# Optimization experiments

Measured on AMD Instinct MI355X. Metric: run time of the kernel, lower is better.

Reference implementation:

```python
import jax, jax.numpy as jnp
import numpy as np

H = 64  # hidden_size
IN = 1  # input_size
OUT = 32  # fc output


def _lstm_layer(x, Wih, Whh, bih, bhh):
    """x: (B,T,D_in). Returns (outputs (B,T,H), final h (B,H)). PyTorch gate order i,f,g,o."""
    B = x.shape[0]
    b = bih + bhh  # (4H,)
    # precompute input contributions for all timesteps: (T,B,4H)
    xW = jnp.einsum('btd,gd->tbg', x, Wih) + b

    def step(carry, xw_t):
        h, c = carry
        gates = xw_t + h @ Whh.T  # (B,4H)
        i, f, g, o = jnp.split(gates, 4, axis=-1)
        i = jax.nn.sigmoid(i)
        f = jax.nn.sigmoid(f)
        g = jnp.tanh(g)
        o = jax.nn.sigmoid(o)
        c = f * c + i * g
        h = o * jnp.tanh(c)
        return (h, c), h

    h0 = jnp.zeros((B, H), dtype=x.dtype)
    c0 = jnp.zeros((B, H), dtype=x.dtype)
    (h_T, _), hs = jax.lax.scan(step, (h0, c0), xW)
    return jnp.swapaxes(hs, 0, 1), h_T


def setup_inputs() -> dict:
    key = jax.random.key(0)
    ks = jax.random.split(key, 11)
    s_ih0 = 1.0 / np.sqrt(H)
    inp = {
        'x': jax.random.normal(ks[0], (2048, 512, IN), dtype=jnp.float32),
        # layer 0: input_size -> H
        'Wih0': jax.random.uniform(ks[1], (4 * H, IN), minval=-s_ih0, maxval=s_ih0),
        'Whh0': jax.random.uniform(ks[2], (4 * H, H), minval=-s_ih0, maxval=s_ih0),
        'bih0': jax.random.uniform(ks[3], (4 * H,), minval=-s_ih0, maxval=s_ih0),
        'bhh0': jax.random.uniform(ks[4], (4 * H,), minval=-s_ih0, maxval=s_ih0),
        # layer 1: H -> H
        'Wih1': jax.random.uniform(ks[5], (4 * H, H), minval=-s_ih0, maxval=s_ih0),
        'Whh1': jax.random.uniform(ks[6], (4 * H, H), minval=-s_ih0, maxval=s_ih0),
        'bih1': jax.random.uniform(ks[7], (4 * H,), minval=-s_ih0, maxval=s_ih0),
        'bhh1': jax.random.uniform(ks[8], (4 * H,), minval=-s_ih0, maxval=s_ih0),
        # fc: H -> 32
        'fcW': jax.random.uniform(ks[9], (OUT, H), minval=-s_ih0, maxval=s_ih0),
        'fcb': jax.random.uniform(ks[10], (OUT,), minval=-s_ih0, maxval=s_ih0),
    }
    return inp


def reference(x, Wih0, Whh0, bih0, bhh0, Wih1, Whh1, bih1, bhh1, fcW, fcb):
    h1_seq, _ = _lstm_layer(x, Wih0, Whh0, bih0, bhh0)
    _, h_last = _lstm_layer(h1_seq, Wih1, Whh1, bih1, bhh1)  # hidden[-1]
    features = jax.nn.relu(h_last @ fcW.T + fcb)  # (B, 32)
    return features
```

## Files before the change

### kernel.cpp

```cpp
#include <hip/hip_runtime.h>
#include <hip/hip_bf16.h>


#define HID 64
#define TSTEPS 512
#define MB 8
#define RS 80

typedef _Float16 f16x8 __attribute__((ext_vector_type(8)));
typedef float f32x4 __attribute__((ext_vector_type(4)));
typedef float f32x2 __attribute__((ext_vector_type(2)));

#define KSIG (-1.44269504089f)
#define KTANH (2.88539008178f)

__device__ __forceinline__ f32x2 mk2(float a, float b) { f32x2 r; r[0] = a; r[1] = b; return r; }
__device__ __forceinline__ f32x2 exp2v(f32x2 v) {
    f32x2 r; r[0] = __builtin_amdgcn_exp2f(v[0]); r[1] = __builtin_amdgcn_exp2f(v[1]); return r;
}
__device__ __forceinline__ f32x2 rcpv(f32x2 v) {
    f32x2 r; r[0] = __builtin_amdgcn_rcpf(v[0]); r[1] = __builtin_amdgcn_rcpf(v[1]); return r;
}
__device__ __forceinline__ f32x2 sig2(f32x2 p)  { return rcpv(exp2v(p) + 1.0f); }
__device__ __forceinline__ f32x2 tanh2(f32x2 p) { return 1.0f - 2.0f * rcpv(exp2v(p) + 1.0f); }

__global__ __launch_bounds__(512, 1) void lstm_feat_kernel(
    const float* __restrict__ x,
    const float* __restrict__ Wih0, const float* __restrict__ Whh0,
    const float* __restrict__ bih0, const float* __restrict__ bhh0,
    const float* __restrict__ Wih1, const float* __restrict__ Whh1,
    const float* __restrict__ bih1, const float* __restrict__ bhh1,
    const float* __restrict__ fcW, const float* __restrict__ fcb,
    float* __restrict__ out)
{
    __shared__ float x_lds[(MB / 2) * TSTEPS * 2];
    __shared__ __align__(16) _Float16 h0_lds[2][MB * RS];
    __shared__ __align__(16) _Float16 h1_lds[2][MB * RS];
    __shared__ float h1f32[MB * HID];
    __shared__ float fcw_lds[HID * 32];
    __shared__ float fcb_lds[32];

    const int tid  = threadIdx.x;
    const int wave = tid >> 6;
    const int lane = tid & 63;
    const int nq   = lane & 15;
    const int quad = lane >> 4;
    const int bbase = blockIdx.x * MB;
    const bool isL1 = (wave >= 4);
    const int ug = wave & 3;
    const int u  = ug * 16 + nq;

    for (int i = tid; i < TSTEPS * MB; i += 512) {
        int r = i >> 9, t = i & (TSTEPS - 1);
        x_lds[(r >> 1) * (TSTEPS * 2) + t * 2 + (r & 1)] = x[(bbase + r) * TSTEPS + t];
    }
    for (int i = tid; i < 32 * HID; i += 512) {
        int o = i >> 6, kk = i & 63;
        fcw_lds[kk * 32 + o] = fcW[i];
    }
    if (tid < 32) fcb_lds[tid] = fcb[tid];
    for (int i = tid; i < 2 * MB * RS; i += 512) {
        ((_Float16*)h0_lds)[i] = (_Float16)0.f;
        ((_Float16*)h1_lds)[i] = (_Float16)0.f;
    }

    f16x8 wA[4][2], wB[4][2];
    f32x4 cbias[4];
    float wx0s[4];
    {
        const float* Wa = isL1 ? Wih1 : Whh0;
        const float* Wb = isL1 ? Whh1 : Whh0;
        const float* bi = isL1 ? bih1 : bih0;
        const float* bh = isL1 ? bhh1 : bhh0;
        #pragma unroll
        for (int g = 0; g < 4; ++g) {
            const float sc = (g == 2) ? KTANH : KSIG;
            const int n = g * 64 + u;
            const float bs = (bi[n] + bh[n]) * sc;
            cbias[g] = (f32x4){bs, bs, bs, bs};
            wx0s[g] = Wih0[n] * sc;
            #pragma unroll
            for (int ks = 0; ks < 2; ++ks) {
                const int k0 = quad * 8 + ks * 32;
                f16x8 a, b;
                #pragma unroll
                for (int j = 0; j < 8; ++j) {
                    a[j] = (_Float16)(Wa[n * HID + k0 + j] * sc);
                    b[j] = (_Float16)(Wb[n * HID + k0 + j] * sc);
                }
                wA[g][ks] = a; wB[g][ks] = b;
            }
        }
    }

    const f32x4 zero4 = {0.f, 0.f, 0.f, 0.f};
    const int arow = (nq >> 1) * RS + quad * 8;
    const int b0r  = (quad * 2) * RS;
    const int hbase = quad * 2;
    f32x2 cc = mk2(0.f, 0.f);

    __syncthreads();

#define L0_SUB(P, Q, XQ2) do {                                                       \
    f16x8 a0_ = *(const f16x8*)&h0_lds[P][arow];                                     \
    f16x8 a1_ = *(const f16x8*)&h0_lds[P][arow + 32];                                \
    f32x4 ac[4];                                                                     \
    __builtin_amdgcn_s_setprio(1);                                                   \
    _Pragma("unroll")                                                                \
    for (int g = 0; g < 4; ++g)                                                      \
        ac[g] = __builtin_amdgcn_mfma_f32_16x16x32_f16(a0_, wA[g][0], cbias[g], 0, 0, 0); \
    _Pragma("unroll")                                                                \
    for (int g = 0; g < 4; ++g)                                                      \
        ac[g] = __builtin_amdgcn_mfma_f32_16x16x32_f16(a1_, wA[g][1], ac[g], 0, 0, 0); \
    __builtin_amdgcn_s_setprio(0);                                                   \
    f32x2 pi = (XQ2) * wx0s[0] + mk2(ac[0][0], ac[0][2]);                            \
    f32x2 pf = (XQ2) * wx0s[1] + mk2(ac[1][0], ac[1][2]);                            \
    f32x2 pg = (XQ2) * wx0s[2] + mk2(ac[2][0], ac[2][2]);                            \
    f32x2 po = (XQ2) * wx0s[3] + mk2(ac[3][0], ac[3][2]);                            \
    f32x2 iv = sig2(pi), fv = sig2(pf), gv = tanh2(pg), ov = sig2(po);               \
    cc = fv * cc + iv * gv;                                                          \
    f32x2 hh = ov * tanh2(cc * KTANH);                                               \
    h0_lds[Q][b0r + u]      = (_Float16)hh[0];                                       \
    h0_lds[Q][b0r + RS + u] = (_Float16)hh[1];                                       \
} while (0)

#define L1_SUB(P, Q, GUARD) do {                                                     \
    f16x8 a00 = *(const f16x8*)&h0_lds[P][arow];                                     \
    f16x8 a01 = *(const f16x8*)&h0_lds[P][arow + 32];                                \
    f16x8 a10 = *(const f16x8*)&h1_lds[P][arow];                                     \
    f16x8 a11 = *(const f16x8*)&h1_lds[P][arow + 32];                                \
    f32x4 aA[4], aB[4];                                                              \
    __builtin_amdgcn_s_setprio(1);                                                   \
    _Pragma("unroll")                                                                \
    for (int g = 0; g < 4; ++g)                                                      \
        aA[g] = __builtin_amdgcn_mfma_f32_16x16x32_f16(a00, wA[g][0], zero4, 0, 0, 0); \
    _Pragma("unroll")                                                                \
    for (int g = 0; g < 4; ++g)                                                      \
        aB[g] = __builtin_amdgcn_mfma_f32_16x16x32_f16(a10, wB[g][0], cbias[g], 0, 0, 0); \
    _Pragma("unroll")                                                                \
    for (int g = 0; g < 4; ++g)                                                      \
        aA[g] = __builtin_amdgcn_mfma_f32_16x16x32_f16(a01, wA[g][1], aA[g], 0, 0, 0); \
    _Pragma("unroll")                                                                \
    for (int g = 0; g < 4; ++g)                                                      \
        aB[g] = __builtin_amdgcn_mfma_f32_16x16x32_f16(a11, wB[g][1], aB[g], 0, 0, 0); \
    __builtin_amdgcn_s_setprio(0);                                                   \
    if (GUARD) {                                                                     \
        f32x2 pi = mk2(aA[0][0], aA[0][2]) + mk2(aB[0][0], aB[0][2]);                \
        f32x2 pf = mk2(aA[1][0], aA[1][2]) + mk2(aB[1][0], aB[1][2]);                \
        f32x2 pg = mk2(aA[2][0], aA[2][2]) + mk2(aB[2][0], aB[2][2]);                \
        f32x2 po = mk2(aA[3][0], aA[3][2]) + mk2(aB[3][0], aB[3][2]);                \
        f32x2 iv = sig2(pi), fv = sig2(pf), gv = tanh2(pg), ov = sig2(po);           \
        cc = fv * cc + iv * gv;                                                      \
        f32x2 hh = ov * tanh2(cc * KTANH);                                           \
        h1_lds[Q][b0r + u]      = (_Float16)hh[0];                                   \
        h1_lds[Q][b0r + RS + u] = (_Float16)hh[1];                                   \
    }                                                                                \
} while (0)

    const int xoff = quad * (TSTEPS * 2);
    for (int k = 0; k < TSTEPS; k += 2) {
        f32x2 xa, xb;
        if (!isL1) {
            const f32x4 xv = *(const f32x4*)&x_lds[xoff + k * 2];
            xa = mk2(xv[0], xv[1]); xb = mk2(xv[2], xv[3]);
            L0_SUB(0, 1, xa);
        } else {
            L1_SUB(0, 1, (k > 0));
        }
        __syncthreads();
        if (!isL1) {
            L0_SUB(1, 0, xb);
        } else {
            L1_SUB(1, 0, true);
        }
        __syncthreads();
    }

    if (isL1) {
        f16x8 a00 = *(const f16x8*)&h0_lds[0][arow];
        f16x8 a01 = *(const f16x8*)&h0_lds[0][arow + 32];
        f16x8 a10 = *(const f16x8*)&h1_lds[0][arow];
        f16x8 a11 = *(const f16x8*)&h1_lds[0][arow + 32];
        f32x4 aA[4], aB[4];
        #pragma unroll
        for (int g = 0; g < 4; ++g)
            aA[g] = __builtin_amdgcn_mfma_f32_16x16x32_f16(a00, wA[g][0], zero4, 0, 0, 0);
        #pragma unroll
        for (int g = 0; g < 4; ++g)
            aB[g] = __builtin_amdgcn_mfma_f32_16x16x32_f16(a10, wB[g][0], cbias[g], 0, 0, 0);
        #pragma unroll
        for (int g = 0; g < 4; ++g)
            aA[g] = __builtin_amdgcn_mfma_f32_16x16x32_f16(a01, wA[g][1], aA[g], 0, 0, 0);
        #pragma unroll
        for (int g = 0; g < 4; ++g)
            aB[g] = __builtin_amdgcn_mfma_f32_16x16x32_f16(a11, wB[g][1], aB[g], 0, 0, 0);
        f32x2 pi = mk2(aA[0][0], aA[0][2]) + mk2(aB[0][0], aB[0][2]);
        f32x2 pf = mk2(aA[1][0], aA[1][2]) + mk2(aB[1][0], aB[1][2]);
        f32x2 pg = mk2(aA[2][0], aA[2][2]) + mk2(aB[2][0], aB[2][2]);
        f32x2 po = mk2(aA[3][0], aA[3][2]) + mk2(aB[3][0], aB[3][2]);
        f32x2 iv = sig2(pi), fv = sig2(pf), gv = tanh2(pg), ov = sig2(po);
        cc = fv * cc + iv * gv;
        f32x2 hh = ov * tanh2(cc * KTANH);
        h1f32[hbase * HID + u]       = hh[0];
        h1f32[(hbase + 1) * HID + u] = hh[1];
    }
    __syncthreads();

    if (tid < MB * 32) {
        const int o  = tid & 31;
        const int rr = tid >> 5;
        float acc = fcb_lds[o];
        #pragma unroll 8
        for (int kk = 0; kk < HID; ++kk)
            acc += h1f32[rr * HID + kk] * fcw_lds[kk * 32 + o];
        out[(bbase + rr) * 32 + o] = fmaxf(acc, 0.f);
    }
}

extern "C" void kernel_launch(void* const* d_in, const int* in_sizes, int n_in,
                              void* d_out, int out_size, void* d_ws, size_t ws_size,
                              hipStream_t stream) {
    const float* x    = (const float*)d_in[0];
    const float* Wih0 = (const float*)d_in[1];
    const float* Whh0 = (const float*)d_in[2];
    const float* bih0 = (const float*)d_in[3];
    const float* bhh0 = (const float*)d_in[4];
    const float* Wih1 = (const float*)d_in[5];
    const float* Whh1 = (const float*)d_in[6];
    const float* bih1 = (const float*)d_in[7];
    const float* bhh1 = (const float*)d_in[8];
    const float* fcW  = (const float*)d_in[9];
    const float* fcb  = (const float*)d_in[10];
    float* out = (float*)d_out;

    lstm_feat_kernel<<<2048 / MB, 512, 0, stream>>>(
        x, Wih0, Whh0, bih0, bhh0, Wih1, Whh1, bih1, bhh1, fcW, fcb, out);
}
```

Before: 316.0 us.

## Lag layer-1 by two steps and precompute its input projection off the critical path

Layer 1 now runs two timesteps behind layer 0, with a four-deep h0 ring buffer. The Wih1·h0 projection for a later step is computed after the recurrent MFMAs and carried in accumulator registers, so only the Whh1 chain sits on the dependent path. Layer 0 folds the x·Wih0 term into the MFMA accumulator init instead of adding it afterwards, and the loop is unrolled by four with scalar activations. In exchange it uses more LDS and accumulator registers and needs extra prologue and epilogue steps to drain the lag.

Result: no change. 312.7 us (-1.0%).

```diff
diff --git a/kernel.cpp b/kernel.cpp
--- a/kernel.cpp
+++ b/kernel.cpp
@@ -9,20 +9,16 @@
 
 typedef _Float16 f16x8 __attribute__((ext_vector_type(8)));
 typedef float f32x4 __attribute__((ext_vector_type(4)));
-typedef float f32x2 __attribute__((ext_vector_type(2)));
 
 #define KSIG (-1.44269504089f)
 #define KTANH (2.88539008178f)
 
-__device__ __forceinline__ f32x2 mk2(float a, float b) { f32x2 r; r[0] = a; r[1] = b; return r; }
-__device__ __forceinline__ f32x2 exp2v(f32x2 v) {
-    f32x2 r; r[0] = __builtin_amdgcn_exp2f(v[0]); r[1] = __builtin_amdgcn_exp2f(v[1]); return r;
-}
-__device__ __forceinline__ f32x2 rcpv(f32x2 v) {
-    f32x2 r; r[0] = __builtin_amdgcn_rcpf(v[0]); r[1] = __builtin_amdgcn_rcpf(v[1]); return r;
-}
-__device__ __forceinline__ f32x2 sig2(f32x2 p)  { return rcpv(exp2v(p) + 1.0f); }
-__device__ __forceinline__ f32x2 tanh2(f32x2 p) { return 1.0f - 2.0f * rcpv(exp2v(p) + 1.0f); }
+__device__ __forceinline__ float sig1(float p) {
+    return __builtin_amdgcn_rcpf(1.f + __builtin_amdgcn_exp2f(p));
+}
+__device__ __forceinline__ float th1(float p) {
+    return 1.f - 2.f * __builtin_amdgcn_rcpf(1.f + __builtin_amdgcn_exp2f(p));
+}
 
 __global__ __launch_bounds__(512, 1) void lstm_feat_kernel(
     const float* __restrict__ x,
@@ -34,7 +30,7 @@
     float* __restrict__ out)
 {
     __shared__ float x_lds[(MB / 2) * TSTEPS * 2];
-    __shared__ __align__(16) _Float16 h0_lds[2][MB * RS];
+    __shared__ __align__(16) _Float16 h0_lds[4][MB * RS];
     __shared__ __align__(16) _Float16 h1_lds[2][MB * RS];
     __shared__ float h1f32[MB * HID];
     __shared__ float fcw_lds[HID * 32];
@@ -59,14 +55,12 @@
         fcw_lds[kk * 32 + o] = fcW[i];
     }
     if (tid < 32) fcb_lds[tid] = fcb[tid];
-    for (int i = tid; i < 2 * MB * RS; i += 512) {
-        ((_Float16*)h0_lds)[i] = (_Float16)0.f;
-        ((_Float16*)h1_lds)[i] = (_Float16)0.f;
-    }
+    for (int i = tid; i < 4 * MB * RS; i += 512) ((_Float16*)h0_lds)[i] = (_Float16)0.f;
+    for (int i = tid; i < 2 * MB * RS; i += 512) ((_Float16*)h1_lds)[i] = (_Float16)0.f;
 
     f16x8 wA[4][2], wB[4][2];
     f32x4 cbias[4];
-    float wx0s[4];
+    float bsc[4], wx0s[4];
     {
         const float* Wa = isL1 ? Wih1 : Whh0;
         const float* Wb = isL1 ? Whh1 : Whh0;
@@ -77,6 +71,7 @@
             const float sc = (g == 2) ? KTANH : KSIG;
             const int n = g * 64 + u;
             const float bs = (bi[n] + bh[n]) * sc;
+            bsc[g] = bs;
             cbias[g] = (f32x4){bs, bs, bs, bs};
             wx0s[g] = Wih0[n] * sc;
             #pragma unroll
@@ -93,116 +88,145 @@
         }
     }
 
-    const f32x4 zero4 = {0.f, 0.f, 0.f, 0.f};
     const int arow = (nq >> 1) * RS + quad * 8;
     const int b0r  = (quad * 2) * RS;
     const int hbase = quad * 2;
-    f32x2 cc = mk2(0.f, 0.f);
+    float c0 = 0.f, c1 = 0.f;
+    f32x4 accA[4] = { {0,0,0,0},{0,0,0,0},{0,0,0,0},{0,0,0,0} };
 
     __syncthreads();
 
-#define L0_SUB(P, Q, XQ2) do {                                                       \
-    f16x8 a0_ = *(const f16x8*)&h0_lds[P][arow];                                     \
-    f16x8 a1_ = *(const f16x8*)&h0_lds[P][arow + 32];                                \
-    f32x4 ac[4];                                                                     \
-    __builtin_amdgcn_s_setprio(1);                                                   \
-    _Pragma("unroll")                                                                \
-    for (int g = 0; g < 4; ++g)                                                      \
-        ac[g] = __builtin_amdgcn_mfma_f32_16x16x32_f16(a0_, wA[g][0], cbias[g], 0, 0, 0); \
-    _Pragma("unroll")                                                                \
-    for (int g = 0; g < 4; ++g)                                                      \
-        ac[g] = __builtin_amdgcn_mfma_f32_16x16x32_f16(a1_, wA[g][1], ac[g], 0, 0, 0); \
-    __builtin_amdgcn_s_setprio(0);                                                   \
-    f32x2 pi = (XQ2) * wx0s[0] + mk2(ac[0][0], ac[0][2]);                            \
-    f32x2 pf = (XQ2) * wx0s[1] + mk2(ac[1][0], ac[1][2]);                            \
-    f32x2 pg = (XQ2) * wx0s[2] + mk2(ac[2][0], ac[2][2]);                            \
-    f32x2 po = (XQ2) * wx0s[3] + mk2(ac[3][0], ac[3][2]);                            \
-    f32x2 iv = sig2(pi), fv = sig2(pf), gv = tanh2(pg), ov = sig2(po);               \
-    cc = fv * cc + iv * gv;                                                          \
-    f32x2 hh = ov * tanh2(cc * KTANH);                                               \
-    h0_lds[Q][b0r + u]      = (_Float16)hh[0];                                       \
-    h0_lds[Q][b0r + RS + u] = (_Float16)hh[1];                                       \
-} while (0)
-
-#define L1_SUB(P, Q, GUARD) do {                                                     \
-    f16x8 a00 = *(const f16x8*)&h0_lds[P][arow];                                     \
-    f16x8 a01 = *(const f16x8*)&h0_lds[P][arow + 32];                                \
-    f16x8 a10 = *(const f16x8*)&h1_lds[P][arow];                                     \
-    f16x8 a11 = *(const f16x8*)&h1_lds[P][arow + 32];                                \
-    f32x4 aA[4], aB[4];                                                              \
-    __builtin_amdgcn_s_setprio(1);                                                   \
-    _Pragma("unroll")                                                                \
-    for (int g = 0; g < 4; ++g)                                                      \
-        aA[g] = __builtin_amdgcn_mfma_f32_16x16x32_f16(a00, wA[g][0], zero4, 0, 0, 0); \
-    _Pragma("unroll")                                                                \
-    for (int g = 0; g < 4; ++g)                                                      \
-        aB[g] = __builtin_amdgcn_mfma_f32_16x16x32_f16(a10, wB[g][0], cbias[g], 0, 0, 0); \
-    _Pragma("unroll")                                                                \
-    for (int g = 0; g < 4; ++g)                                                      \
-        aA[g] = __builtin_amdgcn_mfma_f32_16x16x32_f16(a01, wA[g][1], aA[g], 0, 0, 0); \
-    _Pragma("unroll")                                                                \
-    for (int g = 0; g < 4; ++g)                                                      \
-        aB[g] = __builtin_amdgcn_mfma_f32_16x16x32_f16(a11, wB[g][1], aB[g], 0, 0, 0); \
-    __builtin_amdgcn_s_setprio(0);                                                   \
-    if (GUARD) {                                                                     \
-        f32x2 pi = mk2(aA[0][0], aA[0][2]) + mk2(aB[0][0], aB[0][2]);                \
-        f32x2 pf = mk2(aA[1][0], aA[1][2]) + mk2(aB[1][0], aB[1][2]);                \
-        f32x2 pg = mk2(aA[2][0], aA[2][2]) + mk2(aB[2][0], aB[2][2]);                \
-        f32x2 po = mk2(aA[3][0], aA[3][2]) + mk2(aB[3][0], aB[3][2]);                \
-        f32x2 iv = sig2(pi), fv = sig2(pf), gv = tanh2(pg), ov = sig2(po);           \
-        cc = fv * cc + iv * gv;                                                      \
-        f32x2 hh = ov * tanh2(cc * KTANH);                                           \
-        h1_lds[Q][b0r + u]      = (_Float16)hh[0];                                   \
-        h1_lds[Q][b0r + RS + u] = (_Float16)hh[1];                                   \
-    }                                                                                \
+#define CELL(AC, DST) do {                                                        \
+    float i0 = sig1(AC[0][0]), i1 = sig1(AC[0][2]);                               \
+    float f0 = sig1(AC[1][0]), f1 = sig1(AC[1][2]);                               \
+    float g0 = th1(AC[2][0]),  g1 = th1(AC[2][2]);                                \
+    float o0 = sig1(AC[3][0]), o1 = sig1(AC[3][2]);                               \
+    c0 = f0 * c0 + i0 * g0;  c1 = f1 * c1 + i1 * g1;                              \
+    float t0 = th1(c0 * KTANH), t1 = th1(c1 * KTANH);                             \
+    (DST)[b0r + u]      = (_Float16)(o0 * t0);                                    \
+    (DST)[b0r + RS + u] = (_Float16)(o1 * t1);                                    \
+} while (0)
+
+#define L0_STEP(P, Q, XA, XB) do {                                                \
+    f16x8 a0 = *(const f16x8*)&h0_lds[P][arow];                                   \
+    f16x8 a1 = *(const f16x8*)&h0_lds[P][arow + 32];                              \
+    f32x4 ac[4];                                                                  \
+    __builtin_amdgcn_s_setprio(1);                                                \
+    _Pragma("unroll")                                                             \
+    for (int g = 0; g < 4; ++g) {                                                 \
+        f32x4 Cg;                                                                 \
+        Cg[0] = fmaf((XA), wx0s[g], bsc[g]); Cg[1] = bsc[g];                      \
+        Cg[2] = fmaf((XB), wx0s[g], bsc[g]); Cg[3] = bsc[g];                      \
+        ac[g] = __builtin_amdgcn_mfma_f32_16x16x32_f16(a0, wA[g][0], Cg, 0, 0, 0);\
+    }                                                                             \
+    _Pragma("unroll")                                                             \
+    for (int g = 0; g < 4; ++g)                                                   \
+        ac[g] = __builtin_amdgcn_mfma_f32_16x16x32_f16(a1, wA[g][1], ac[g], 0, 0, 0); \
+    __builtin_amdgcn_s_setprio(0);                                                \
+    CELL(ac, h0_lds[Q]);                                                          \
+} while (0)
+
+#define L1_STEP(RB, WRB, PF) do {                                                 \
+    f16x8 b0v = *(const f16x8*)&h1_lds[RB][arow];                                 \
+    f16x8 b1v = *(const f16x8*)&h1_lds[RB][arow + 32];                            \
+    f16x8 p0 = *(const f16x8*)&h0_lds[PF][arow];                                  \
+    f16x8 p1 = *(const f16x8*)&h0_lds[PF][arow + 32];                             \
+    f32x4 ac[4];                                                                  \
+    __builtin_amdgcn_s_setprio(1);                                                \
+    _Pragma("unroll")                                                             \
+    for (int g = 0; g < 4; ++g)                                                   \
+        ac[g] = __builtin_amdgcn_mfma_f32_16x16x32_f16(b0v, wB[g][0], accA[g], 0, 0, 0); \
+    _Pragma("unroll")                                                             \
+    for (int g = 0; g < 4; ++g)                                                   \
+        ac[g] = __builtin_amdgcn_mfma_f32_16x16x32_f16(b1v, wB[g][1], ac[g], 0, 0, 0);   \
+    __builtin_amdgcn_s_setprio(0);                                                \
+    _Pragma("unroll")                                                             \
+    for (int g = 0; g < 4; ++g)                                                   \
+        accA[g] = __builtin_amdgcn_mfma_f32_16x16x32_f16(p0, wA[g][0], cbias[g], 0, 0, 0); \
+    _Pragma("unroll")                                                             \
+    for (int g = 0; g < 4; ++g)                                                   \
+        accA[g] = __builtin_amdgcn_mfma_f32_16x16x32_f16(p1, wA[g][1], accA[g], 0, 0, 0);  \
+    CELL(ac, h1_lds[WRB]);                                                        \
+} while (0)
+
+#define L1_PF(PF) do {                                                            \
+    f16x8 p0 = *(const f16x8*)&h0_lds[PF][arow];                                  \
+    f16x8 p1 = *(const f16x8*)&h0_lds[PF][arow + 32];                             \
+    _Pragma("unroll")                                                             \
+    for (int g = 0; g < 4; ++g)                                                   \
+        accA[g] = __builtin_amdgcn_mfma_f32_16x16x32_f16(p0, wA[g][0], cbias[g], 0, 0, 0); \
+    _Pragma("unroll")                                                             \
+    for (int g = 0; g < 4; ++g)                                                   \
+        accA[g] = __builtin_amdgcn_mfma_f32_16x16x32_f16(p1, wA[g][1], accA[g], 0, 0, 0);  \
 } while (0)
 
     const int xoff = quad * (TSTEPS * 2);
-    for (int k = 0; k < TSTEPS; k += 2) {
-        f32x2 xa, xb;
-        if (!isL1) {
-            const f32x4 xv = *(const f32x4*)&x_lds[xoff + k * 2];
-            xa = mk2(xv[0], xv[1]); xb = mk2(xv[2], xv[3]);
-            L0_SUB(0, 1, xa);
-        } else {
-            L1_SUB(0, 1, (k > 0));
-        }
-        __syncthreads();
-        if (!isL1) {
-            L0_SUB(1, 0, xb);
-        } else {
-            L1_SUB(1, 0, true);
-        }
+
+    {
+        const f32x4 xv0 = *(const f32x4*)&x_lds[xoff + 0];
+        const f32x4 xv1 = *(const f32x4*)&x_lds[xoff + 4];
+        if (!isL1) L0_STEP(0, 1, xv0[0], xv0[1]); else L1_PF(0);
+        __syncthreads();
+        if (!isL1) L0_STEP(1, 2, xv0[2], xv0[3]); else L1_PF(1);
+        __syncthreads();
+        if (!isL1) L0_STEP(2, 3, xv1[0], xv1[1]); else L1_STEP(0, 1, 2);
+        __syncthreads();
+        if (!isL1) L0_STEP(3, 0, xv1[2], xv1[3]); else L1_STEP(1, 0, 3);
+        __syncthreads();
+    }
+
+    for (int k = 4; k < TSTEPS; k += 4) {
+        const f32x4 xv0 = *(const f32x4*)&x_lds[xoff + k * 2];
+        const f32x4 xv1 = *(const f32x4*)&x_lds[xoff + k * 2 + 4];
+        if (!isL1) L0_STEP(0, 1, xv0[0], xv0[1]); else L1_STEP(0, 1, 0);
+        __syncthreads();
+        if (!isL1) L0_STEP(1, 2, xv0[2], xv0[3]); else L1_STEP(1, 0, 1);
+        __syncthreads();
+        if (!isL1) L0_STEP(2, 3, xv1[0], xv1[1]); else L1_STEP(0, 1, 2);
+        __syncthreads();
+        if (!isL1) L0_STEP(3, 0, xv1[2], xv1[3]); else L1_STEP(1, 0, 3);
         __syncthreads();
     }
 
     if (isL1) {
-        f16x8 a00 = *(const f16x8*)&h0_lds[0][arow];
-        f16x8 a01 = *(const f16x8*)&h0_lds[0][arow + 32];
-        f16x8 a10 = *(const f16x8*)&h1_lds[0][arow];
-        f16x8 a11 = *(const f16x8*)&h1_lds[0][arow + 32];
-        f32x4 aA[4], aB[4];
-        #pragma unroll
-        for (int g = 0; g < 4; ++g)
-            aA[g] = __builtin_amdgcn_mfma_f32_16x16x32_f16(a00, wA[g][0], zero4, 0, 0, 0);
-        #pragma unroll
-        for (int g = 0; g < 4; ++g)
-            aB[g] = __builtin_amdgcn_mfma_f32_16x16x32_f16(a10, wB[g][0], cbias[g], 0, 0, 0);
-        #pragma unroll
-        for (int g = 0; g < 4; ++g)
-            aA[g] = __builtin_amdgcn_mfma_f32_16x16x32_f16(a01, wA[g][1], aA[g], 0, 0, 0);
-        #pragma unroll
-        for (int g = 0; g < 4; ++g)
-            aB[g] = __builtin_amdgcn_mfma_f32_16x16x32_f16(a11, wB[g][1], aB[g], 0, 0, 0);
-        f32x2 pi = mk2(aA[0][0], aA[0][2]) + mk2(aB[0][0], aB[0][2]);
-        f32x2 pf = mk2(aA[1][0], aA[1][2]) + mk2(aB[1][0], aB[1][2]);
-        f32x2 pg = mk2(aA[2][0], aA[2][2]) + mk2(aB[2][0], aB[2][2]);
-        f32x2 po = mk2(aA[3][0], aA[3][2]) + mk2(aB[3][0], aB[3][2]);
-        f32x2 iv = sig2(pi), fv = sig2(pf), gv = tanh2(pg), ov = sig2(po);
-        cc = fv * cc + iv * gv;
-        f32x2 hh = ov * tanh2(cc * KTANH);
-        h1f32[hbase * HID + u]       = hh[0];
-        h1f32[(hbase + 1) * HID + u] = hh[1];
+        f16x8 b0v = *(const f16x8*)&h1_lds[0][arow];
+        f16x8 b1v = *(const f16x8*)&h1_lds[0][arow + 32];
+        f32x4 ac[4];
+        #pragma unroll
+        for (int g = 0; g < 4; ++g)
+            ac[g] = __builtin_amdgcn_mfma_f32_16x16x32_f16(b0v, wB[g][0], accA[g], 0, 0, 0);
+        #pragma unroll
+        for (int g = 0; g < 4; ++g)
+            ac[g] = __builtin_amdgcn_mfma_f32_16x16x32_f16(b1v, wB[g][1], ac[g], 0, 0, 0);
+        CELL(ac, h1_lds[1]);
+    }
+    __syncthreads();
+
+    if (isL1) {
+        f16x8 p0  = *(const f16x8*)&h0_lds[0][arow];
+        f16x8 p1  = *(const f16x8*)&h0_lds[0][arow + 32];
+        f16x8 b0v = *(const f16x8*)&h1_lds[1][arow];
+        f16x8 b1v = *(const f16x8*)&h1_lds[1][arow + 32];
+        f32x4 ac[4];
+        #pragma unroll
+        for (int g = 0; g < 4; ++g)
+            ac[g] = __builtin_amdgcn_mfma_f32_16x16x32_f16(p0, wA[g][0], cbias[g], 0, 0, 0);
+        #pragma unroll
+        for (int g = 0; g < 4; ++g)
+            ac[g] = __builtin_amdgcn_mfma_f32_16x16x32_f16(p1, wA[g][1], ac[g], 0, 0, 0);
+        #pragma unroll
+        for (int g = 0; g < 4; ++g)
+            ac[g] = __builtin_amdgcn_mfma_f32_16x16x32_f16(b0v, wB[g][0], ac[g], 0, 0, 0);
+        #pragma unroll
+        for (int g = 0; g < 4; ++g)
+            ac[g] = __builtin_amdgcn_mfma_f32_16x16x32_f16(b1v, wB[g][1], ac[g], 0, 0, 0);
+        float i0 = sig1(ac[0][0]), i1 = sig1(ac[0][2]);
+        float f0 = sig1(ac[1][0]), f1 = sig1(ac[1][2]);
+        float g0 = th1(ac[2][0]),  g1 = th1(ac[2][2]);
+        float o0 = sig1(ac[3][0]), o1 = sig1(ac[3][2]);
+        c0 = f0 * c0 + i0 * g0;  c1 = f1 * c1 + i1 * g1;
+        h1f32[hbase * HID + u]       = o0 * th1(c0 * KTANH);
+        h1f32[(hbase + 1) * HID + u] = o1 * th1(c1 * KTANH);
     }
     __syncthreads();
 
```

## Replace block barriers with LDS counter spin-waits and deeper h0 ring buffer

Applied to the files above, without the earlier changes.

Removes the two __syncthreads per timestep pair and instead has each wave publish its completed step into an LDS counter array. Waves spin on the minimum counters of the layer-0 and layer-1 groups. Layer 0 gets a 4-deep h0 ring buffer so it can run up to a few steps ahead of layer 1, which now processes timestep k-1 in a wavefront-skewed pipeline. Layer 1's MFMA chains are merged into a single accumulator, and the gate math is rewritten in scalar fmaf form. The intent is to cut barrier stalls and let the two layers overlap more loosely, at the cost of spin-polling LDS and relying on fences for correct ordering.

After: 435.4 us. 1.38x slower.

```diff
diff --git a/kernel.cpp b/kernel.cpp
--- a/kernel.cpp
+++ b/kernel.cpp
@@ -9,20 +9,17 @@
 
 typedef _Float16 f16x8 __attribute__((ext_vector_type(8)));
 typedef float f32x4 __attribute__((ext_vector_type(4)));
-typedef float f32x2 __attribute__((ext_vector_type(2)));
 
 #define KSIG (-1.44269504089f)
 #define KTANH (2.88539008178f)
 
-__device__ __forceinline__ f32x2 mk2(float a, float b) { f32x2 r; r[0] = a; r[1] = b; return r; }
-__device__ __forceinline__ f32x2 exp2v(f32x2 v) {
-    f32x2 r; r[0] = __builtin_amdgcn_exp2f(v[0]); r[1] = __builtin_amdgcn_exp2f(v[1]); return r;
-}
-__device__ __forceinline__ f32x2 rcpv(f32x2 v) {
-    f32x2 r; r[0] = __builtin_amdgcn_rcpf(v[0]); r[1] = __builtin_amdgcn_rcpf(v[1]); return r;
-}
-__device__ __forceinline__ f32x2 sig2(f32x2 p)  { return rcpv(exp2v(p) + 1.0f); }
-__device__ __forceinline__ f32x2 tanh2(f32x2 p) { return 1.0f - 2.0f * rcpv(exp2v(p) + 1.0f); }
+__device__ __forceinline__ float sig1(float p) {
+    return __builtin_amdgcn_rcpf(1.f + __builtin_amdgcn_exp2f(p));
+}
+__device__ __forceinline__ float th1(float p) {
+    return 1.f - 2.f * __builtin_amdgcn_rcpf(1.f + __builtin_amdgcn_exp2f(p));
+}
+__device__ __forceinline__ int imin(int a, int b) { return a < b ? a : b; }
 
 __global__ __launch_bounds__(512, 1) void lstm_feat_kernel(
     const float* __restrict__ x,
@@ -33,12 +30,13 @@
     const float* __restrict__ fcW, const float* __restrict__ fcb,
     float* __restrict__ out)
 {
-    __shared__ float x_lds[(MB / 2) * TSTEPS * 2];
-    __shared__ __align__(16) _Float16 h0_lds[2][MB * RS];
+    __shared__ __align__(16) float x_lds[(MB / 2) * TSTEPS * 2];
+    __shared__ __align__(16) _Float16 h0_lds[4][MB * RS];
     __shared__ __align__(16) _Float16 h1_lds[2][MB * RS];
     __shared__ float h1f32[MB * HID];
     __shared__ float fcw_lds[HID * 32];
     __shared__ float fcb_lds[32];
+    __shared__ int cnt[8];
 
     const int tid  = threadIdx.x;
     const int wave = tid >> 6;
@@ -59,17 +57,16 @@
         fcw_lds[kk * 32 + o] = fcW[i];
     }
     if (tid < 32) fcb_lds[tid] = fcb[tid];
-    for (int i = tid; i < 2 * MB * RS; i += 512) {
-        ((_Float16*)h0_lds)[i] = (_Float16)0.f;
-        ((_Float16*)h1_lds)[i] = (_Float16)0.f;
-    }
+    for (int i = tid; i < 4 * MB * RS; i += 512) ((_Float16*)h0_lds)[i] = (_Float16)0.f;
+    for (int i = tid; i < 2 * MB * RS; i += 512) ((_Float16*)h1_lds)[i] = (_Float16)0.f;
+    if (tid < 4) cnt[tid] = -1;
+    else if (tid < 8) cnt[tid] = 0;
 
     f16x8 wA[4][2], wB[4][2];
     f32x4 cbias[4];
     float wx0s[4];
     {
         const float* Wa = isL1 ? Wih1 : Whh0;
-        const float* Wb = isL1 ? Whh1 : Whh0;
         const float* bi = isL1 ? bih1 : bih0;
         const float* bh = isL1 ? bhh1 : bhh0;
         #pragma unroll
@@ -82,127 +79,160 @@
             #pragma unroll
             for (int ks = 0; ks < 2; ++ks) {
                 const int k0 = quad * 8 + ks * 32;
-                f16x8 a, b;
+                f16x8 a;
                 #pragma unroll
-                for (int j = 0; j < 8; ++j) {
+                for (int j = 0; j < 8; ++j)
                     a[j] = (_Float16)(Wa[n * HID + k0 + j] * sc);
-                    b[j] = (_Float16)(Wb[n * HID + k0 + j] * sc);
+                wA[g][ks] = a;
+            }
+        }
+        if (isL1) {
+            #pragma unroll
+            for (int g = 0; g < 4; ++g) {
+                const float sc = (g == 2) ? KTANH : KSIG;
+                const int n = g * 64 + u;
+                #pragma unroll
+                for (int ks = 0; ks < 2; ++ks) {
+                    const int k0 = quad * 8 + ks * 32;
+                    f16x8 b;
+                    #pragma unroll
+                    for (int j = 0; j < 8; ++j)
+                        b[j] = (_Float16)(Whh1[n * HID + k0 + j] * sc);
+                    wB[g][ks] = b;
                 }
-                wA[g][ks] = a; wB[g][ks] = b;
             }
         }
     }
 
-    const f32x4 zero4 = {0.f, 0.f, 0.f, 0.f};
     const int arow = (nq >> 1) * RS + quad * 8;
     const int b0r  = (quad * 2) * RS;
     const int hbase = quad * 2;
-    f32x2 cc = mk2(0.f, 0.f);
+    float c0 = 0.f, c1 = 0.f;
 
     __syncthreads();
 
-#define L0_SUB(P, Q, XQ2) do {                                                       \
-    f16x8 a0_ = *(const f16x8*)&h0_lds[P][arow];                                     \
-    f16x8 a1_ = *(const f16x8*)&h0_lds[P][arow + 32];                                \
-    f32x4 ac[4];                                                                     \
-    __builtin_amdgcn_s_setprio(1);                                                   \
-    _Pragma("unroll")                                                                \
-    for (int g = 0; g < 4; ++g)                                                      \
-        ac[g] = __builtin_amdgcn_mfma_f32_16x16x32_f16(a0_, wA[g][0], cbias[g], 0, 0, 0); \
-    _Pragma("unroll")                                                                \
-    for (int g = 0; g < 4; ++g)                                                      \
-        ac[g] = __builtin_amdgcn_mfma_f32_16x16x32_f16(a1_, wA[g][1], ac[g], 0, 0, 0); \
-    __builtin_amdgcn_s_setprio(0);                                                   \
-    f32x2 pi = (XQ2) * wx0s[0] + mk2(ac[0][0], ac[0][2]);                            \
-    f32x2 pf = (XQ2) * wx0s[1] + mk2(ac[1][0], ac[1][2]);                            \
-    f32x2 pg = (XQ2) * wx0s[2] + mk2(ac[2][0], ac[2][2]);                            \
-    f32x2 po = (XQ2) * wx0s[3] + mk2(ac[3][0], ac[3][2]);                            \
-    f32x2 iv = sig2(pi), fv = sig2(pf), gv = tanh2(pg), ov = sig2(po);               \
-    cc = fv * cc + iv * gv;                                                          \
-    f32x2 hh = ov * tanh2(cc * KTANH);                                               \
-    h0_lds[Q][b0r + u]      = (_Float16)hh[0];                                       \
-    h0_lds[Q][b0r + RS + u] = (_Float16)hh[1];                                       \
-} while (0)
-
-#define L1_SUB(P, Q, GUARD) do {                                                     \
-    f16x8 a00 = *(const f16x8*)&h0_lds[P][arow];                                     \
-    f16x8 a01 = *(const f16x8*)&h0_lds[P][arow + 32];                                \
-    f16x8 a10 = *(const f16x8*)&h1_lds[P][arow];                                     \
-    f16x8 a11 = *(const f16x8*)&h1_lds[P][arow + 32];                                \
-    f32x4 aA[4], aB[4];                                                              \
-    __builtin_amdgcn_s_setprio(1);                                                   \
-    _Pragma("unroll")                                                                \
-    for (int g = 0; g < 4; ++g)                                                      \
-        aA[g] = __builtin_amdgcn_mfma_f32_16x16x32_f16(a00, wA[g][0], zero4, 0, 0, 0); \
-    _Pragma("unroll")                                                                \
-    for (int g = 0; g < 4; ++g)                                                      \
-        aB[g] = __builtin_amdgcn_mfma_f32_16x16x32_f16(a10, wB[g][0], cbias[g], 0, 0, 0); \
-    _Pragma("unroll")                                                                \
-    for (int g = 0; g < 4; ++g)                                                      \
-        aA[g] = __builtin_amdgcn_mfma_f32_16x16x32_f16(a01, wA[g][1], aA[g], 0, 0, 0); \
-    _Pragma("unroll")                                                                \
-    for (int g = 0; g < 4; ++g)                                                      \
-        aB[g] = __builtin_amdgcn_mfma_f32_16x16x32_f16(a11, wB[g][1], aB[g], 0, 0, 0); \
-    __builtin_amdgcn_s_setprio(0);                                                   \
-    if (GUARD) {                                                                     \
-        f32x2 pi = mk2(aA[0][0], aA[0][2]) + mk2(aB[0][0], aB[0][2]);                \
-        f32x2 pf = mk2(aA[1][0], aA[1][2]) + mk2(aB[1][0], aB[1][2]);                \
-        f32x2 pg = mk2(aA[2][0], aA[2][2]) + mk2(aB[2][0], aB[2][2]);                \
-        f32x2 po = mk2(aA[3][0], aA[3][2]) + mk2(aB[3][0], aB[3][2]);                \
-        f32x2 iv = sig2(pi), fv = sig2(pf), gv = tanh2(pg), ov = sig2(po);           \
-        cc = fv * cc + iv * gv;                                                      \
-        f32x2 hh = ov * tanh2(cc * KTANH);                                           \
-        h1_lds[Q][b0r + u]      = (_Float16)hh[0];                                   \
-        h1_lds[Q][b0r + RS + u] = (_Float16)hh[1];                                   \
-    }                                                                                \
+#define SPIN(N0, N1) do {                                                        \
+    volatile int* cv = cnt;                                                      \
+    for (;;) {                                                                   \
+        int m0 = imin(imin(cv[0], cv[1]), imin(cv[2], cv[3]));                   \
+        int m1 = imin(imin(cv[4], cv[5]), imin(cv[6], cv[7]));                   \
+        if (m0 >= (N0) && m1 >= (N1)) break;                                     \
+        __builtin_amdgcn_s_sleep(1);                                             \
+    }                                                                            \
+    asm volatile("" ::: "memory");                                               \
+} while (0)
+
+#define PUBLISH(V) do {                                                          \
+    __threadfence_block();                                                       \
+    if (lane == 0) ((volatile int*)cnt)[wave] = (V);                             \
+} while (0)
+
+#define L0_ONE(J, P, Q, XA, XB) do {                                             \
+    SPIN((J) - 1, (J) - 3);                                                      \
+    f16x8 a0 = *(const f16x8*)&h0_lds[P][arow];                                  \
+    f16x8 a1 = *(const f16x8*)&h0_lds[P][arow + 32];                             \
+    f32x4 ac[4];                                                                 \
+    __builtin_amdgcn_s_setprio(1);                                               \
+    _Pragma("unroll")                                                            \
+    for (int g = 0; g < 4; ++g)                                                  \
+        ac[g] = __builtin_amdgcn_mfma_f32_16x16x32_f16(a0, wA[g][0], cbias[g], 0, 0, 0); \
+    _Pragma("unroll")                                                            \
+    for (int g = 0; g < 4; ++g)                                                  \
+        ac[g] = __builtin_amdgcn_mfma_f32_16x16x32_f16(a1, wA[g][1], ac[g], 0, 0, 0);    \
+    __builtin_amdgcn_s_setprio(0);                                               \
+    float pi0 = fmaf((XA), wx0s[0], ac[0][0]), pi1 = fmaf((XB), wx0s[0], ac[0][2]); \
+    float pf0 = fmaf((XA), wx0s[1], ac[1][0]), pf1 = fmaf((XB), wx0s[1], ac[1][2]); \
+    float pg0 = fmaf((XA), wx0s[2], ac[2][0]), pg1 = fmaf((XB), wx0s[2], ac[2][2]); \
+    float po0 = fmaf((XA), wx0s[3], ac[3][0]), po1 = fmaf((XB), wx0s[3], ac[3][2]); \
+    float iv0 = sig1(pi0), iv1 = sig1(pi1);                                      \
+    float fv0 = sig1(pf0), fv1 = sig1(pf1);                                      \
+    float gv0 = th1(pg0),  gv1 = th1(pg1);                                       \
+    float ov0 = sig1(po0), ov1 = sig1(po1);                                      \
+    c0 = fmaf(fv0, c0, iv0 * gv0);  c1 = fmaf(fv1, c1, iv1 * gv1);               \
+    h0_lds[Q][b0r + u]      = (_Float16)(ov0 * th1(c0 * KTANH));                 \
+    h0_lds[Q][b0r + RS + u] = (_Float16)(ov1 * th1(c1 * KTANH));                 \
+    PUBLISH(J);                                                                  \
+} while (0)
+
+#define L1_ONE(K, PH, RB, WB) do {                                               \
+    SPIN((K) - 1, (K) - 1);                                                      \
+    f16x8 a00 = *(const f16x8*)&h0_lds[PH][arow];                                \
+    f16x8 a01 = *(const f16x8*)&h0_lds[PH][arow + 32];                           \
+    f16x8 a10 = *(const f16x8*)&h1_lds[RB][arow];                                \
+    f16x8 a11 = *(const f16x8*)&h1_lds[RB][arow + 32];                           \
+    f32x4 ac[4];                                                                 \
+    __builtin_amdgcn_s_setprio(1);                                               \
+    _Pragma("unroll")                                                            \
+    for (int g = 0; g < 4; ++g)                                                  \
+        ac[g] = __builtin_amdgcn_mfma_f32_16x16x32_f16(a00, wA[g][0], cbias[g], 0, 0, 0); \
+    _Pragma("unroll")                                                            \
+    for (int g = 0; g < 4; ++g)                                                  \
+        ac[g] = __builtin_amdgcn_mfma_f32_16x16x32_f16(a01, wA[g][1], ac[g], 0, 0, 0);   \
+    _Pragma("unroll")                                                            \
+    for (int g = 0; g < 4; ++g)                                                  \
+        ac[g] = __builtin_amdgcn_mfma_f32_16x16x32_f16(a10, wB[g][0], ac[g], 0, 0, 0);   \
+    _Pragma("unroll")                                                            \
+    for (int g = 0; g < 4; ++g)                                                  \
+        ac[g] = __builtin_amdgcn_mfma_f32_16x16x32_f16(a11, wB[g][1], ac[g], 0, 0, 0);   \
+    __builtin_amdgcn_s_setprio(0);                                               \
+    float iv0 = sig1(ac[0][0]), iv1 = sig1(ac[0][2]);                            \
+    float fv0 = sig1(ac[1][0]), fv1 = sig1(ac[1][2]);                            \
+    float gv0 = th1(ac[2][0]),  gv1 = th1(ac[2][2]);                             \
+    float ov0 = sig1(ac[3][0]), ov1 = sig1(ac[3][2]);                            \
+    c0 = fmaf(fv0, c0, iv0 * gv0);  c1 = fmaf(fv1, c1, iv1 * gv1);               \
+    h1_lds[WB][b0r + u]      = (_Float16)(ov0 * th1(c0 * KTANH));                \
+    h1_lds[WB][b0r + RS + u] = (_Float16)(ov1 * th1(c1 * KTANH));                \
+    PUBLISH(K);                                                                  \
 } while (0)
 
     const int xoff = quad * (TSTEPS * 2);
-    for (int k = 0; k < TSTEPS; k += 2) {
-        f32x2 xa, xb;
-        if (!isL1) {
-            const f32x4 xv = *(const f32x4*)&x_lds[xoff + k * 2];
-            xa = mk2(xv[0], xv[1]); xb = mk2(xv[2], xv[3]);
-            L0_SUB(0, 1, xa);
-        } else {
-            L1_SUB(0, 1, (k > 0));
-        }
-        __syncthreads();
-        if (!isL1) {
-            L0_SUB(1, 0, xb);
-        } else {
-            L1_SUB(1, 0, true);
-        }
-        __syncthreads();
-    }
-
-    if (isL1) {
-        f16x8 a00 = *(const f16x8*)&h0_lds[0][arow];
-        f16x8 a01 = *(const f16x8*)&h0_lds[0][arow + 32];
-        f16x8 a10 = *(const f16x8*)&h1_lds[0][arow];
-        f16x8 a11 = *(const f16x8*)&h1_lds[0][arow + 32];
-        f32x4 aA[4], aB[4];
-        #pragma unroll
-        for (int g = 0; g < 4; ++g)
-            aA[g] = __builtin_amdgcn_mfma_f32_16x16x32_f16(a00, wA[g][0], zero4, 0, 0, 0);
-        #pragma unroll
-        for (int g = 0; g < 4; ++g)
-            aB[g] = __builtin_amdgcn_mfma_f32_16x16x32_f16(a10, wB[g][0], cbias[g], 0, 0, 0);
-        #pragma unroll
-        for (int g = 0; g < 4; ++g)
-            aA[g] = __builtin_amdgcn_mfma_f32_16x16x32_f16(a01, wA[g][1], aA[g], 0, 0, 0);
-        #pragma unroll
-        for (int g = 0; g < 4; ++g)
-            aB[g] = __builtin_amdgcn_mfma_f32_16x16x32_f16(a11, wB[g][1], aB[g], 0, 0, 0);
-        f32x2 pi = mk2(aA[0][0], aA[0][2]) + mk2(aB[0][0], aB[0][2]);
-        f32x2 pf = mk2(aA[1][0], aA[1][2]) + mk2(aB[1][0], aB[1][2]);
-        f32x2 pg = mk2(aA[2][0], aA[2][2]) + mk2(aB[2][0], aB[2][2]);
-        f32x2 po = mk2(aA[3][0], aA[3][2]) + mk2(aB[3][0], aB[3][2]);
-        f32x2 iv = sig2(pi), fv = sig2(pf), gv = tanh2(pg), ov = sig2(po);
-        cc = fv * cc + iv * gv;
-        f32x2 hh = ov * tanh2(cc * KTANH);
-        h1f32[hbase * HID + u]       = hh[0];
-        h1f32[(hbase + 1) * HID + u] = hh[1];
+
+    if (!isL1) {
+        for (int j4 = 0; j4 < TSTEPS; j4 += 4) {
+            const f32x4 xva = *(const f32x4*)&x_lds[xoff + j4 * 2];
+            const f32x4 xvb = *(const f32x4*)&x_lds[xoff + j4 * 2 + 4];
+            L0_ONE(j4 + 0, 0, 1, xva[0], xva[1]);
+            L0_ONE(j4 + 1, 1, 2, xva[2], xva[3]);
+            L0_ONE(j4 + 2, 2, 3, xvb[0], xvb[1]);
+            L0_ONE(j4 + 3, 3, 0, xvb[2], xvb[3]);
+        }
+    } else {
+        for (int k4 = 1; k4 <= TSTEPS - 7; k4 += 4) {
+            L1_ONE(k4 + 0, 1, 0, 1);
+            L1_ONE(k4 + 1, 2, 1, 0);
+            L1_ONE(k4 + 2, 3, 0, 1);
+            L1_ONE(k4 + 3, 0, 1, 0);
+        }
+        L1_ONE(509, 1, 0, 1);
+        L1_ONE(510, 2, 1, 0);
+        L1_ONE(511, 3, 0, 1);
+        {
+            SPIN(511, 511);
+            f16x8 a00 = *(const f16x8*)&h0_lds[0][arow];
+            f16x8 a01 = *(const f16x8*)&h0_lds[0][arow + 32];
+            f16x8 a10 = *(const f16x8*)&h1_lds[1][arow];
+            f16x8 a11 = *(const f16x8*)&h1_lds[1][arow + 32];
+            f32x4 ac[4];
+            #pragma unroll
+            for (int g = 0; g < 4; ++g)
+                ac[g] = __builtin_amdgcn_mfma_f32_16x16x32_f16(a00, wA[g][0], cbias[g], 0, 0, 0);
+            #pragma unroll
+            for (int g = 0; g < 4; ++g)
+                ac[g] = __builtin_amdgcn_mfma_f32_16x16x32_f16(a01, wA[g][1], ac[g], 0, 0, 0);
+            #pragma unroll
+            for (int g = 0; g < 4; ++g)
+                ac[g] = __builtin_amdgcn_mfma_f32_16x16x32_f16(a10, wB[g][0], ac[g], 0, 0, 0);
+            #pragma unroll
+            for (int g = 0; g < 4; ++g)
+                ac[g] = __builtin_amdgcn_mfma_f32_16x16x32_f16(a11, wB[g][1], ac[g], 0, 0, 0);
+            float iv0 = sig1(ac[0][0]), iv1 = sig1(ac[0][2]);
+            float fv0 = sig1(ac[1][0]), fv1 = sig1(ac[1][2]);
+            float gv0 = th1(ac[2][0]),  gv1 = th1(ac[2][2]);
+            float ov0 = sig1(ac[3][0]), ov1 = sig1(ac[3][2]);
+            c0 = fmaf(fv0, c0, iv0 * gv0);  c1 = fmaf(fv1, c1, iv1 * gv1);
+            h1f32[hbase * HID + u]       = ov0 * th1(c0 * KTANH);
+            h1f32[(hbase + 1) * HID + u] = ov1 * th1(c1 * KTANH);
+        }
     }
     __syncthreads();
 
```
